# Kernel tuning notes

Hardware: AMD Instinct MI355X
Metric: run time of the kernel (lower is better)

The kernel has to match this reference:

```python
import jax, jax.numpy as jnp
import numpy as np
from jax import lax

BLANK = 27
NEG = -1e30  # safe -inf substitute (avoids NaN grads through logaddexp)


def _joint_log_probs(enc, dec, We, Wd, bf, Wp, bp):
    # Concat-then-Linear == sum of per-branch matmuls: [e;d] @ Wf = e@We + d@Wd.
    f = jnp.einsum('bte,eh->bth', enc, We)          # [B,T,H]
    g = jnp.einsum('bud,dh->buh', dec, Wd)          # [B,U1,H]
    h = jnp.tanh(f[:, :, None, :] + g[:, None, :, :] + bf)  # [B,T,U1,H]
    logits = jnp.einsum('btuh,hv->btuv', h, Wp) + bp         # [B,T,U1,V]
    return jax.nn.log_softmax(logits, axis=-1)


def _rnnt_loss_one(lp, tgt, t_len, u_len):
    # lp: [T,U1,V] log-probs, tgt: [U] int labels, t_len/u_len: scalars.
    T, U1, V = lp.shape
    blank_lp = lp[:, :, BLANK]                                   # [T,U1]
    lab_lp = jnp.take_along_axis(lp[:, :U1 - 1, :],
                                 tgt[None, :, None], axis=2)[..., 0]  # [T,U]

    # alpha[0,:] : only label emissions along u at t=0.
    alpha0 = jnp.concatenate([jnp.zeros((1,), lp.dtype),
                              jnp.cumsum(lab_lp[0])])            # [U1]

    def step(prev_alpha, inp):
        b_prev, lab_t = inp                       # [U1], [U]
        from_below = prev_alpha + b_prev          # blank move from t-1
        first = from_below[0]

        def inner(carry, x):
            fb, lab = x
            new = jnp.logaddexp(fb, carry + lab)  # blank-from-below vs label-from-left
            return new, new

        _, rest = lax.scan(inner, first, (from_below[1:], lab_t))
        alpha_t = jnp.concatenate([first[None], rest])
        return alpha_t, alpha_t

    _, alphas = lax.scan(step, alpha0, (blank_lp[:-1], lab_lp[1:]))
    alpha = jnp.concatenate([alpha0[None], alphas], axis=0)      # [T,U1]

    # Terminal: emit final blank at (t_len-1, u_len).
    return -(alpha[t_len - 1, u_len] + blank_lp[t_len - 1, u_len])


def setup_inputs() -> dict:
    key = jax.random.key(0)
    ks = jax.random.split(key, 10)
    B, T, U, E, D, H, V = 8, 400, 60, 256, 256, 512, 28
    enc_state = jax.random.normal(ks[0], (B, T, E), jnp.float32)
    dec_state = jax.random.normal(ks[1], (B, U + 1, D), jnp.float32)
    targets = jax.random.randint(ks[2], (B, U), 0, BLANK, jnp.int32)
    inputs_length = jax.random.randint(ks[3], (B,), 200, T + 1, jnp.int32)
    targets_length = jax.random.randint(ks[4], (B,), 30, U + 1, jnp.int32)
    s1 = 1.0 / np.sqrt(E + D)
    s2 = 1.0 / np.sqrt(H)
    We = jax.random.normal(ks[5], (E, H), jnp.float32) * s1
    Wd = jax.random.normal(ks[6], (D, H), jnp.float32) * s1
    bf = jax.random.normal(ks[7], (H,), jnp.float32) * s1
    Wp = jax.random.normal(ks[8], (H, V), jnp.float32) * s2
    bp = jax.random.normal(ks[9], (V,), jnp.float32) * s2
    return {"enc_state": enc_state, "dec_state": dec_state,
            "We": We, "Wd": Wd, "bf": bf, "Wp": Wp, "bp": bp,
            "targets": targets, "inputs_length": inputs_length,
            "targets_length": targets_length}


def reference(enc_state, dec_state, We, Wd, bf, Wp, bp,
              targets, inputs_length, targets_length):
    lp = _joint_log_probs(enc_state, dec_state, We, Wd, bf, Wp, bp)
    loss = jax.vmap(_rnnt_loss_one)(lp, targets, inputs_length, targets_length)
    return loss  # [B], reduction='none'
```

## Files before the change

kernel.cpp:

```cpp
#include <hip/hip_runtime.h>
#include <hip/hip_bf16.h>
#include <math.h>

#define NEGF (-1e30f)
#define LOG2E 1.4426950408889634f
#define TSCALE 2.885390081777927f

typedef __attribute__((ext_vector_type(8))) short bf16x8;
typedef __attribute__((ext_vector_type(4))) float f32x4;

#define DROWS_PAD 480
#define DPITCH 64
#define PF 16

__device__ __forceinline__ unsigned short f2bf(float x) {
    __hip_bfloat16 h = __float2bfloat16(x);
    return *reinterpret_cast<unsigned short*>(&h);
}

__device__ __forceinline__ float wave_shr1(float x) {
    int i = __builtin_bit_cast(int, x);
    int r = __builtin_amdgcn_update_dpp(0, i, 0x138, 0xf, 0xf, true);
    return __builtin_bit_cast(float, r);
}

__device__ __forceinline__ float4 rcp4_nr(float4 d) {
    float4 y;
    y.x = __builtin_bit_cast(float, 0x7EF311C3 - __builtin_bit_cast(int, d.x));
    y.y = __builtin_bit_cast(float, 0x7EF311C3 - __builtin_bit_cast(int, d.y));
    y.z = __builtin_bit_cast(float, 0x7EF311C3 - __builtin_bit_cast(int, d.z));
    y.w = __builtin_bit_cast(float, 0x7EF311C3 - __builtin_bit_cast(int, d.w));
    float4 t;
    t.x = fmaf(-d.x, y.x, 2.f); t.y = fmaf(-d.y, y.y, 2.f);
    t.z = fmaf(-d.z, y.z, 2.f); t.w = fmaf(-d.w, y.w, 2.f);
    y.x *= t.x; y.y *= t.y; y.z *= t.z; y.w *= t.w;
    return y;
}

__global__ __launch_bounds__(256) void k_pack(const float* __restrict__ We,
                                              const float* __restrict__ Wd,
                                              const float* __restrict__ Wp,
                                              const float* __restrict__ bp,
                                              unsigned short* __restrict__ WeFrag,
                                              unsigned short* __restrict__ WdFrag,
                                              unsigned short* __restrict__ BfragP,
                                              float* __restrict__ csbp) {
    int gid = blockIdx.x * 256 + threadIdx.x;
    if (gid < 32768) {
        const float* W = (gid < 16384) ? We : Wd;
        unsigned short* F = (gid < 16384) ? WeFrag : WdFrag;
        int s = gid & 16383;
        int lane = s & 63;
        int c = (s >> 6) & 7;
        int nt = s >> 9;
        int n = nt * 16 + (lane & 15);
        int kbase = c * 32 + ((lane >> 4) & 3) * 8;
        unsigned short* dst = F + (size_t)s * 8;
#pragma unroll
        for (int j = 0; j < 8; ++j) dst[j] = f2bf(W[(size_t)(kbase + j) * 512 + n]);
    } else if (gid < 34816) {
        int s = gid - 32768;
        int lane = s & 63;
        int half = (s >> 6) & 1;
        int c = s >> 7;
        int n = half * 16 + (lane & 15);
        int kbase = c * 32 + (lane >> 4) * 8;
        unsigned short* dst = BfragP + (size_t)s * 8;
#pragma unroll
        for (int j = 0; j < 8; ++j) {
            float v = (n < 28) ? (-2.f * Wp[(kbase + j) * 28 + n]) : 0.f;
            dst[j] = f2bf(v);
        }
    } else if (gid < 34848) {
        int v = gid - 34816;
        float s = 0.f;
        if (v < 28) {
            for (int k = 0; k < 512; ++k) s += Wp[k * 28 + v];
            s += bp[v];
        }
        csbp[v] = s;
    }
}

__global__ __launch_bounds__(256) void k_gemm(const float* __restrict__ enc,
                                              const float* __restrict__ dec,
                                              const float* __restrict__ bfv,
                                              const unsigned short* __restrict__ WeFrag,
                                              const unsigned short* __restrict__ WdFrag,
                                              float* __restrict__ f,
                                              float* __restrict__ g) {
    const int wid = blockIdx.x * 4 + threadIdx.y;
    const int lane = threadIdx.x;
    const int m16 = lane & 15;
    const int quad = lane >> 4;

    const float* A; const unsigned short* WF; float* Out; int M, rt, ct; bool isg;
    if (wid < 1600) { A = enc; WF = WeFrag; Out = f; M = 3200; rt = wid >> 3; ct = wid & 7; isg = false; }
    else { int w2 = wid - 1600; A = dec; WF = WdFrag; Out = g; M = 488; rt = w2 >> 3; ct = w2 & 7; isg = true; }

    const int row = rt * 16 + m16;
    const float* arow = A + (size_t)min(row, M - 1) * 256 + quad * 8;

    f32x4 acc[4];
#pragma unroll
    for (int i = 0; i < 4; ++i) acc[i] = (f32x4){0.f, 0.f, 0.f, 0.f};

#pragma unroll
    for (int c = 0; c < 8; ++c) {
        float4 a0 = *(const float4*)(arow + c * 32);
        float4 a1 = *(const float4*)(arow + c * 32 + 4);
        union { unsigned short s[8]; bf16x8 v; } Af;
        Af.s[0] = f2bf(a0.x); Af.s[1] = f2bf(a0.y);
        Af.s[2] = f2bf(a0.z); Af.s[3] = f2bf(a0.w);
        Af.s[4] = f2bf(a1.x); Af.s[5] = f2bf(a1.y);
        Af.s[6] = f2bf(a1.z); Af.s[7] = f2bf(a1.w);
#pragma unroll
        for (int i = 0; i < 4; ++i) {
            int nt = ct * 4 + i;
            bf16x8 Bv = *(const bf16x8*)(WF + (size_t)((nt * 8 + c) * 64 + lane) * 8);
            acc[i] = __builtin_amdgcn_mfma_f32_16x16x32_bf16(Af.v, Bv, acc[i], 0, 0, 0);
        }
    }

#pragma unroll
    for (int i = 0; i < 4; ++i) {
        int n = ct * 64 + i * 16 + m16;
        float bv = isg ? bfv[n] : 0.f;
#pragma unroll
        for (int r = 0; r < 4; ++r) {
            int ro = rt * 16 + quad * 4 + r;
            if (ro < M) Out[(size_t)ro * 512 + n] = (acc[i][r] + bv) * TSCALE;
        }
    }
}

__global__ __launch_bounds__(256) void k_cells(const float* __restrict__ f,
                                               const float* __restrict__ g,
                                               const unsigned short* __restrict__ Bfrag,
                                               const float* __restrict__ csbp,
                                               const int* __restrict__ targets,
                                               const int* __restrict__ ilen,
                                               const int* __restrict__ ulenp,
                                               float2* __restrict__ pairD) {
    const int b = blockIdx.z;
    const int tlen = ilen[b];
    const int t0 = blockIdx.x * 16;
    if (t0 >= tlen) return;
    if ((int)blockIdx.y * 4 > ulenp[b]) return;
    const int wave = threadIdx.y;
    const int lane = threadIdx.x;
    const int u_raw = blockIdx.y * 4 + wave;
    const int u = min(u_raw, 60);
    const int tid = wave * 64 + lane;

    __shared__ float fs[16 * 516];

    {
        const float4* src = (const float4*)(f + (size_t)(b * 400 + t0) * 512);
#pragma unroll
        for (int i = 0; i < 8; ++i) {
            int idx = tid + i * 256;
            int row = idx >> 7;
            int c4 = idx & 127;
            float4 v = src[idx];
            *(float4*)&fs[row * 516 + c4 * 4] = v;
        }
    }
    __syncthreads();

    const int quad = lane >> 4;
    const int m16 = lane & 15;
    const float* gu = g + (size_t)(b * 61 + u) * 512 + quad * 8;
    const float* fsrow = fs + m16 * 516 + quad * 8;
    f32x4 acc0 = {0.f, 0.f, 0.f, 0.f};
    f32x4 acc1 = {0.f, 0.f, 0.f, 0.f};
    const float4 one4 = make_float4(1.f, 1.f, 1.f, 1.f);

#pragma unroll 4
    for (int c = 0; c < 16; ++c) {
        float4 fa = *(const float4*)(fsrow + c * 32);
        float4 fb = *(const float4*)(fsrow + c * 32 + 4);
        float4 ga = *(const float4*)(gu + c * 32);
        float4 gb = *(const float4*)(gu + c * 32 + 4);
        float4 s0 = fa + ga;
        float4 s1 = fb + gb;
        float4 e0, e1;
        e0.x = __builtin_amdgcn_exp2f(s0.x); e0.y = __builtin_amdgcn_exp2f(s0.y);
        e0.z = __builtin_amdgcn_exp2f(s0.z); e0.w = __builtin_amdgcn_exp2f(s0.w);
        e1.x = __builtin_amdgcn_exp2f(s1.x); e1.y = __builtin_amdgcn_exp2f(s1.y);
        e1.z = __builtin_amdgcn_exp2f(s1.z); e1.w = __builtin_amdgcn_exp2f(s1.w);
        float4 r0 = rcp4_nr(e0 + one4);
        float4 r1 = rcp4_nr(e1 + one4);
        union { unsigned short s[8]; bf16x8 v; } A;
        A.s[0] = f2bf(r0.x); A.s[1] = f2bf(r0.y);
        A.s[2] = f2bf(r0.z); A.s[3] = f2bf(r0.w);
        A.s[4] = f2bf(r1.x); A.s[5] = f2bf(r1.y);
        A.s[6] = f2bf(r1.z); A.s[7] = f2bf(r1.w);
        bf16x8 B0 = *(const bf16x8*)(Bfrag + ((size_t)(c * 2 + 0) * 64 + lane) * 8);
        bf16x8 B1 = *(const bf16x8*)(Bfrag + ((size_t)(c * 2 + 1) * 64 + lane) * 8);
        acc0 = __builtin_amdgcn_mfma_f32_16x16x32_bf16(A.v, B0, acc0, 0, 0, 0);
        acc1 = __builtin_amdgcn_mfma_f32_16x16x32_bf16(A.v, B1, acc1, 0, 0, 0);
    }

    float cs0 = csbp[m16];
    int n1 = 16 + m16;
    bool n1v = (n1 < 28);
    float cs1 = csbp[n1 & 31];
    int tv = targets[b * 60 + min(u, 59)];

    float res_blank[4], res_lab[4];
#pragma unroll
    for (int r = 0; r < 4; ++r) {
        float l0 = acc0[r] + cs0;
        float l1 = n1v ? (acc1[r] + cs1) : NEGF;
        float mx = fmaxf(l0, l1);
        mx = fmaxf(mx, __shfl_xor(mx, 1, 64));
        mx = fmaxf(mx, __shfl_xor(mx, 2, 64));
        mx = fmaxf(mx, __shfl_xor(mx, 4, 64));
        mx = fmaxf(mx, __shfl_xor(mx, 8, 64));
        float s = __builtin_amdgcn_exp2f((l0 - mx) * LOG2E) +
                  __builtin_amdgcn_exp2f((l1 - mx) * LOG2E);
        s += __shfl_xor(s, 1, 64);
        s += __shfl_xor(s, 2, 64);
        s += __shfl_xor(s, 4, 64);
        s += __shfl_xor(s, 8, 64);
        float lse = mx + __logf(s);
        int base = lane & 48;
        float labsrc = (tv < 16) ? l0 : l1;
        float labv = __shfl(labsrc, base | (tv & 15), 64);
        float blankv = __shfl(l1, base | 11, 64);
        res_blank[r] = blankv - lse;
        res_lab[r] = labv - lse;
    }

    if (m16 == 0 && u_raw <= 60) {
        float2* Pd = pairD + (size_t)b * (DROWS_PAD * DPITCH);
#pragma unroll
        for (int r = 0; r < 4; ++r) {
            int t = t0 + quad * 4 + r;
            if (t < tlen) {
                int d = t + u;
                float2 pr;
                pr.x = res_blank[r];
                pr.y = (u <= 59) ? res_lab[r] : NEGF;
                Pd[d * DPITCH + u] = pr;
            }
        }
    }
}

__global__ __launch_bounds__(64) void k_alpha(const float2* __restrict__ pairD,
                                              const int* __restrict__ ilen,
                                              const int* __restrict__ ulenp,
                                              float* __restrict__ out) {
    const int b = blockIdx.x;
    const int u = threadIdx.x;
    const float2* Pd = pairD + (size_t)b * (DROWS_PAD * DPITCH);
    const int tl = ilen[b];
    const int ul = ulenp[b];
    const int dstar = tl - 1 + ul;
    const int dmax = ((dstar + PF - 1) / PF) * PF;
    const bool uok = (u <= 60);
    const bool lok = (u >= 1 && u <= 60);

    float cur = (u == 0) ? 0.f : NEGF;
    float saved = NEGF;

    float2 pf[PF];
#pragma unroll
    for (int i = 0; i < PF; ++i) pf[i] = Pd[i * DPITCH + u];

    for (int d0 = 1; d0 <= dmax; d0 += PF) {
#pragma unroll
        for (int i = 0; i < PF; ++i) {
            const int d = d0 + i;
            float2 v = pf[i];
            pf[i] = Pd[(d + PF - 1) * DPITCH + u];
            int t = d - u;
            float bv = (t >= 1 && t <= 399 && uok) ? v.x : NEGF;
            float lvn = wave_shr1(v.y);
            float lv = (lok && t >= 0 && t <= 399) ? lvn : NEGF;
            float up = wave_shr1(cur);
            float a = cur + bv;
            float c2 = up + lv;
            float mx = fmaxf(a, c2), mn = fminf(a, c2);
            float nv = mx + __logf(1.f + __builtin_amdgcn_exp2f((mn - mx) * LOG2E));
            bool valid = (t >= 0 && t <= 399 && uok);
            cur = valid ? nv : cur;
            saved = (d == dstar) ? cur : saved;
        }
    }
    if (u == ul) out[b] = -(saved + Pd[dstar * DPITCH + u].x);
}

extern "C" void kernel_launch(void* const* d_in, const int* in_sizes, int n_in,
                              void* d_out, int out_size, void* d_ws, size_t ws_size,
                              hipStream_t stream) {
    const float* enc = (const float*)d_in[0];
    const float* dec = (const float*)d_in[1];
    const float* We  = (const float*)d_in[2];
    const float* Wd  = (const float*)d_in[3];
    const float* bf  = (const float*)d_in[4];
    const float* Wp  = (const float*)d_in[5];
    const float* bp  = (const float*)d_in[6];
    const int* targets = (const int*)d_in[7];
    const int* ilen    = (const int*)d_in[8];
    const int* ulen    = (const int*)d_in[9];
    float* out = (float*)d_out;
    float* ws = (float*)d_ws;

    float* f     = ws;
    float* g     = ws + 1638400;
    unsigned short* BfragP = (unsigned short*)(ws + 1888256);
    unsigned short* WeFrag = (unsigned short*)(ws + 1896448);
    unsigned short* WdFrag = (unsigned short*)(ws + 1961984);
    float* csbp  = ws + 2027520;
    float2* pairD = (float2*)(ws + 2027552);

    k_pack<<<137, 256, 0, stream>>>(We, Wd, Wp, bp, WeFrag, WdFrag, BfragP, csbp);

    k_gemm<<<462, dim3(64, 4, 1), 0, stream>>>(enc, dec, bf, WeFrag, WdFrag, f, g);

    dim3 gridC(25, 16, 8);
    dim3 blockC(64, 4, 1);
    k_cells<<<gridC, blockC, 0, stream>>>(f, g, BfragP, csbp, targets, ilen, ulen, pairD);

    k_alpha<<<8, 64, 0, stream>>>(pairD, ilen, ulen, out);
}
```

Measured before the change: 158.3 us.

## Process four u rows per wave in joint kernel and compute in log2 domain

Each wave of k_cells now handles four decoder positions instead of one. The f tile in shared memory and the Wp fragments are reused across all four, and the grid's u dimension shrinks fourfold. The log-softmax and alpha recursion now work in base-2 log space, with a single ln2 rescale at the output. Row reductions use DPP rotates instead of shuffles. The cost is more registers per thread (eight accumulators) and fewer blocks, which could hurt occupancy.

```diff
diff --git a/kernel.cpp b/kernel.cpp
--- a/kernel.cpp
+++ b/kernel.cpp
@@ -4,6 +4,7 @@
 
 #define NEGF (-1e30f)
 #define LOG2E 1.4426950408889634f
+#define LN2F  0.6931471805599453f
 #define TSCALE 2.885390081777927f
 
 typedef __attribute__((ext_vector_type(8))) short bf16x8;
@@ -22,6 +23,19 @@
     int i = __builtin_bit_cast(int, x);
     int r = __builtin_amdgcn_update_dpp(0, i, 0x138, 0xf, 0xf, true);
     return __builtin_bit_cast(float, r);
+}
+
+#define ROR16(x, n) __builtin_bit_cast(float, __builtin_amdgcn_update_dpp( \
+    0, __builtin_bit_cast(int, (x)), 0x120 + (n), 0xf, 0xf, true))
+
+__device__ __forceinline__ float rmax16(float x) {
+    x = fmaxf(x, ROR16(x, 8)); x = fmaxf(x, ROR16(x, 4));
+    x = fmaxf(x, ROR16(x, 2)); x = fmaxf(x, ROR16(x, 1));
+    return x;
+}
+__device__ __forceinline__ float rsum16(float x) {
+    x += ROR16(x, 8); x += ROR16(x, 4); x += ROR16(x, 2); x += ROR16(x, 1);
+    return x;
 }
 
 __device__ __forceinline__ float4 rcp4_nr(float4 d) {
@@ -76,7 +90,7 @@
         float s = 0.f;
         if (v < 28) {
             for (int k = 0; k < 512; ++k) s += Wp[k * 28 + v];
-            s += bp[v];
+            s = (s + bp[v]) * LOG2E;
         }
         csbp[v] = s;
     }
@@ -146,12 +160,11 @@
     const int tlen = ilen[b];
     const int t0 = blockIdx.x * 16;
     if (t0 >= tlen) return;
-    if ((int)blockIdx.y * 4 > ulenp[b]) return;
+    if ((int)blockIdx.y * 16 > ulenp[b]) return;
     const int wave = threadIdx.y;
     const int lane = threadIdx.x;
-    const int u_raw = blockIdx.y * 4 + wave;
-    const int u = min(u_raw, 60);
     const int tid = wave * 64 + lane;
+    const int ubase = blockIdx.y * 16 + wave * 4;
 
     __shared__ float fs[16 * 516];
 
@@ -170,80 +183,84 @@
 
     const int quad = lane >> 4;
     const int m16 = lane & 15;
-    const float* gu = g + (size_t)(b * 61 + u) * 512 + quad * 8;
     const float* fsrow = fs + m16 * 516 + quad * 8;
-    f32x4 acc0 = {0.f, 0.f, 0.f, 0.f};
-    f32x4 acc1 = {0.f, 0.f, 0.f, 0.f};
+    const float* gb0 = g + (size_t)b * 61 * 512 + quad * 8;
+    const float* gu[4];
+    int us[4];
+#pragma unroll
+    for (int uu = 0; uu < 4; ++uu) {
+        us[uu] = min(ubase + uu, 60);
+        gu[uu] = gb0 + (size_t)us[uu] * 512;
+    }
+
+    f32x4 acc[4][2];
+#pragma unroll
+    for (int uu = 0; uu < 4; ++uu) {
+        acc[uu][0] = (f32x4){0.f, 0.f, 0.f, 0.f};
+        acc[uu][1] = (f32x4){0.f, 0.f, 0.f, 0.f};
+    }
     const float4 one4 = make_float4(1.f, 1.f, 1.f, 1.f);
 
-#pragma unroll 4
+#pragma unroll 2
     for (int c = 0; c < 16; ++c) {
         float4 fa = *(const float4*)(fsrow + c * 32);
         float4 fb = *(const float4*)(fsrow + c * 32 + 4);
-        float4 ga = *(const float4*)(gu + c * 32);
-        float4 gb = *(const float4*)(gu + c * 32 + 4);
-        float4 s0 = fa + ga;
-        float4 s1 = fb + gb;
-        float4 e0, e1;
-        e0.x = __builtin_amdgcn_exp2f(s0.x); e0.y = __builtin_amdgcn_exp2f(s0.y);
-        e0.z = __builtin_amdgcn_exp2f(s0.z); e0.w = __builtin_amdgcn_exp2f(s0.w);
-        e1.x = __builtin_amdgcn_exp2f(s1.x); e1.y = __builtin_amdgcn_exp2f(s1.y);
-        e1.z = __builtin_amdgcn_exp2f(s1.z); e1.w = __builtin_amdgcn_exp2f(s1.w);
-        float4 r0 = rcp4_nr(e0 + one4);
-        float4 r1 = rcp4_nr(e1 + one4);
-        union { unsigned short s[8]; bf16x8 v; } A;
-        A.s[0] = f2bf(r0.x); A.s[1] = f2bf(r0.y);
-        A.s[2] = f2bf(r0.z); A.s[3] = f2bf(r0.w);
-        A.s[4] = f2bf(r1.x); A.s[5] = f2bf(r1.y);
-        A.s[6] = f2bf(r1.z); A.s[7] = f2bf(r1.w);
         bf16x8 B0 = *(const bf16x8*)(Bfrag + ((size_t)(c * 2 + 0) * 64 + lane) * 8);
         bf16x8 B1 = *(const bf16x8*)(Bfrag + ((size_t)(c * 2 + 1) * 64 + lane) * 8);
-        acc0 = __builtin_amdgcn_mfma_f32_16x16x32_bf16(A.v, B0, acc0, 0, 0, 0);
-        acc1 = __builtin_amdgcn_mfma_f32_16x16x32_bf16(A.v, B1, acc1, 0, 0, 0);
-    }
-
-    float cs0 = csbp[m16];
-    int n1 = 16 + m16;
-    bool n1v = (n1 < 28);
-    float cs1 = csbp[n1 & 31];
-    int tv = targets[b * 60 + min(u, 59)];
-
-    float res_blank[4], res_lab[4];
-#pragma unroll
-    for (int r = 0; r < 4; ++r) {
-        float l0 = acc0[r] + cs0;
-        float l1 = n1v ? (acc1[r] + cs1) : NEGF;
-        float mx = fmaxf(l0, l1);
-        mx = fmaxf(mx, __shfl_xor(mx, 1, 64));
-        mx = fmaxf(mx, __shfl_xor(mx, 2, 64));
-        mx = fmaxf(mx, __shfl_xor(mx, 4, 64));
-        mx = fmaxf(mx, __shfl_xor(mx, 8, 64));
-        float s = __builtin_amdgcn_exp2f((l0 - mx) * LOG2E) +
-                  __builtin_amdgcn_exp2f((l1 - mx) * LOG2E);
-        s += __shfl_xor(s, 1, 64);
-        s += __shfl_xor(s, 2, 64);
-        s += __shfl_xor(s, 4, 64);
-        s += __shfl_xor(s, 8, 64);
-        float lse = mx + __logf(s);
-        int base = lane & 48;
-        float labsrc = (tv < 16) ? l0 : l1;
-        float labv = __shfl(labsrc, base | (tv & 15), 64);
-        float blankv = __shfl(l1, base | 11, 64);
-        res_blank[r] = blankv - lse;
-        res_lab[r] = labv - lse;
-    }
-
-    if (m16 == 0 && u_raw <= 60) {
-        float2* Pd = pairD + (size_t)b * (DROWS_PAD * DPITCH);
+#pragma unroll
+        for (int uu = 0; uu < 4; ++uu) {
+            float4 ga = *(const float4*)(gu[uu] + c * 32);
+            float4 gb = *(const float4*)(gu[uu] + c * 32 + 4);
+            float4 s0 = fa + ga;
+            float4 s1 = fb + gb;
+            float4 e0, e1;
+            e0.x = __builtin_amdgcn_exp2f(s0.x); e0.y = __builtin_amdgcn_exp2f(s0.y);
+            e0.z = __builtin_amdgcn_exp2f(s0.z); e0.w = __builtin_amdgcn_exp2f(s0.w);
+            e1.x = __builtin_amdgcn_exp2f(s1.x); e1.y = __builtin_amdgcn_exp2f(s1.y);
+            e1.z = __builtin_amdgcn_exp2f(s1.z); e1.w = __builtin_amdgcn_exp2f(s1.w);
+            float4 r0 = rcp4_nr(e0 + one4);
+            float4 r1 = rcp4_nr(e1 + one4);
+            union { unsigned short s[8]; bf16x8 v; } A;
+            A.s[0] = f2bf(r0.x); A.s[1] = f2bf(r0.y);
+            A.s[2] = f2bf(r0.z); A.s[3] = f2bf(r0.w);
+            A.s[4] = f2bf(r1.x); A.s[5] = f2bf(r1.y);
+            A.s[6] = f2bf(r1.z); A.s[7] = f2bf(r1.w);
+            acc[uu][0] = __builtin_amdgcn_mfma_f32_16x16x32_bf16(A.v, B0, acc[uu][0], 0, 0, 0);
+            acc[uu][1] = __builtin_amdgcn_mfma_f32_16x16x32_bf16(A.v, B1, acc[uu][1], 0, 0, 0);
+        }
+    }
+
+    const float cs0 = csbp[m16];
+    const int n1 = 16 + m16;
+    const bool n1v = (n1 < 28);
+    const float cs1 = csbp[n1 & 31];
+    const int base = lane & 48;
+    float2* Pd = pairD + (size_t)b * (DROWS_PAD * DPITCH);
+
+#pragma unroll
+    for (int uu = 0; uu < 4; ++uu) {
+        const int u = us[uu];
+        const int tv = targets[b * 60 + min(u, 59)];
 #pragma unroll
         for (int r = 0; r < 4; ++r) {
-            int t = t0 + quad * 4 + r;
-            if (t < tlen) {
-                int d = t + u;
-                float2 pr;
-                pr.x = res_blank[r];
-                pr.y = (u <= 59) ? res_lab[r] : NEGF;
-                Pd[d * DPITCH + u] = pr;
+            float l0 = fmaf(acc[uu][0][r], LOG2E, cs0);
+            float l1 = n1v ? fmaf(acc[uu][1][r], LOG2E, cs1) : NEGF;
+            float mx = rmax16(fmaxf(l0, l1));
+            float s = __builtin_amdgcn_exp2f(l0 - mx) +
+                      __builtin_amdgcn_exp2f(l1 - mx);
+            s = rsum16(s);
+            float lse = mx + __builtin_amdgcn_logf(s);
+            float labsrc = (tv < 16) ? l0 : l1;
+            float labv = __shfl(labsrc, base | (tv & 15), 64);
+            float blankv = __shfl(l1, base | 11, 64);
+            if (m16 == 0 && ubase + uu <= 60) {
+                int t = t0 + quad * 4 + r;
+                if (t < tlen) {
+                    float2 pr;
+                    pr.x = blankv - lse;
+                    pr.y = (u <= 59) ? (labv - lse) : NEGF;
+                    Pd[(t + u) * DPITCH + u] = pr;
+                }
             }
         }
     }
@@ -284,13 +301,13 @@
             float a = cur + bv;
             float c2 = up + lv;
             float mx = fmaxf(a, c2), mn = fminf(a, c2);
-            float nv = mx + __logf(1.f + __builtin_amdgcn_exp2f((mn - mx) * LOG2E));
+            float nv = mx + __builtin_amdgcn_logf(1.f + __builtin_amdgcn_exp2f(mn - mx));
             bool valid = (t >= 0 && t <= 399 && uok);
             cur = valid ? nv : cur;
             saved = (d == dstar) ? cur : saved;
         }
     }
-    if (u == ul) out[b] = -(saved + Pd[dstar * DPITCH + u].x);
+    if (u == ul) out[b] = -(saved + Pd[dstar * DPITCH + u].x) * LN2F;
 }
 
 extern "C" void kernel_launch(void* const* d_in, const int* in_sizes, int n_in,
@@ -321,7 +338,7 @@
 
     k_gemm<<<462, dim3(64, 4, 1), 0, stream>>>(enc, dec, bf, WeFrag, WdFrag, f, g);
 
-    dim3 gridC(25, 16, 8);
+    dim3 gridC(25, 4, 8);
     dim3 blockC(64, 4, 1);
     k_cells<<<gridC, blockC, 0, stream>>>(f, g, BfragP, csbp, targets, ilen, ulen, pairD);
 
```

After: 160.7 us. Within noise of the previous version (+1.5%).
